# Performance work log

Hardware: AMD Instinct MI355X
Metric: run time of the kernel (lower is better)

## Reference

```python
import jax, jax.numpy as jnp
import numpy as np
import math

DIM = 147      # input feature dim
EMB = 64       # in_dim * head_cnt
M = 32         # int(EMB * kernel_ratio)
EPS_LN = 1e-5
EPS = 1e-8


def layer_norm(x, g, b, eps=EPS_LN):
    mu = jnp.mean(x, axis=-1, keepdims=True)
    var = jnp.mean(jnp.square(x - mu), axis=-1, keepdims=True)
    return (x - mu) * jax.lax.rsqrt(var + eps) * g + b


def prm_exp(x, W_rf):
    # x: [b, t, e], W_rf: [m, e]
    xd = 0.5 * jnp.sum(x * x, axis=-1, keepdims=True)        # [b, t, 1]
    wtx = jnp.einsum('bte,me->btm', x, W_rf)                  # [b, t, m]
    return jnp.exp(wtx - xd) / math.sqrt(M)


def setup_inputs() -> dict:
    key = jax.random.key(0)
    ks = jax.random.split(key, 16)
    B, T = 32, 3136
    s_in = 1.0 / math.sqrt(DIM)
    s_emb = 1.0 / math.sqrt(EMB)
    inp = {
        'x':      jax.random.normal(ks[0], (B, T, DIM), jnp.float32),
        'w_kqv':  jax.random.uniform(ks[1], (3 * EMB, DIM), jnp.float32, -s_in, s_in),
        'b_kqv':  jax.random.uniform(ks[2], (3 * EMB,), jnp.float32, -s_in, s_in),
        'w_proj': jax.random.uniform(ks[3], (EMB, EMB), jnp.float32, -s_emb, s_emb),
        'b_proj': jax.random.uniform(ks[4], (EMB,), jnp.float32, -s_emb, s_emb),
        'g1':     jnp.ones((DIM,), jnp.float32),
        'beta1':  jnp.zeros((DIM,), jnp.float32),
        'g2':     jnp.ones((EMB,), jnp.float32),
        'beta2':  jnp.zeros((EMB,), jnp.float32),
        'w_m1':   jax.random.uniform(ks[5], (EMB, EMB), jnp.float32, -s_emb, s_emb),
        'b_m1':   jax.random.uniform(ks[6], (EMB,), jnp.float32, -s_emb, s_emb),
        'w_m2':   jax.random.uniform(ks[7], (EMB, EMB), jnp.float32, -s_emb, s_emb),
        'b_m2':   jax.random.uniform(ks[8], (EMB,), jnp.float32, -s_emb, s_emb),
        # orthogonal random-feature matrix scaled by sqrt(m) (buffer 'w')
        'W_rf':   jnp.asarray(np.linalg.qr(np.random.RandomState(0).randn(EMB, EMB))[0][:M] * math.sqrt(M), jnp.float32),
    }
    return inp


def reference(x, w_kqv, b_kqv, w_proj, b_proj, g1, beta1, g2, beta2,
              w_m1, b_m1, w_m2, b_m2, W_rf):
    # --- single_attn(norm1(x)) ---
    xn = layer_norm(x, g1, beta1)
    kqv = xn @ w_kqv.T + b_kqv                                  # [b, t, 3e]
    k, q, v = jnp.split(kqv, 3, axis=-1)
    kp = prm_exp(k, W_rf)                                       # [b, t, m]
    qp = prm_exp(q, W_rf)                                       # [b, t, m]
    D = jnp.einsum('btm,bm->bt', qp, kp.sum(axis=1))[..., None]  # [b, t, 1]
    kptv = jnp.einsum('bte,btm->bem', v, kp)                    # [b, e, m]
    y = jnp.einsum('btm,bem->bte', qp, kptv) / (D + EPS)        # [b, t, e]
    y = v + (y @ w_proj.T + b_proj)                             # residual on v
    # --- y + mlp(norm2(y)) ---
    yn = layer_norm(y, g2, beta2)
    h = jax.nn.gelu(yn @ w_m1.T + b_m1, approximate=False)
    out = y + (h @ w_m2.T + b_m2)
    return out
```

## Files before the change

### kernel.cpp

```cpp
#include <hip/hip_runtime.h>
#include <hip/hip_bf16.h>

#define BB 32
#define TT 3136
#define DD 147
#define EE 64
#define MM 32
#define BT (BB*TT)

typedef __hip_bfloat16 bf16;
typedef __attribute__((ext_vector_type(8))) short s8v;
typedef __attribute__((ext_vector_type(4))) float f4v;

__device__ __forceinline__ float b2f(bf16 v){ return __bfloat162float(v); }
__device__ __forceinline__ bf16 f2b(float v){ return __float2bfloat16(v); }
__device__ __forceinline__ unsigned pack2(float a, float b){
  union { bf16 h[2]; unsigned u; } cv; cv.h[0]=f2b(a); cv.h[1]=f2b(b); return cv.u;
}

template<typename T>
__device__ __forceinline__ float cvt1(T v);
template<> __device__ __forceinline__ float cvt1<float>(float v){ return v; }
template<> __device__ __forceinline__ float cvt1<bf16>(bf16 v){ return __bfloat162float(v); }

__device__ __forceinline__ int bf16flag(const void* g1){
  return (*(const unsigned*)g1 == 0x3F803F80u) ? 1 : 0;
}

template<typename T>
__device__ void cvt_body(int idx,
    const T* wkqv, const T* bkqv, const T* Wrf, const T* wproj, const T* bproj,
    const T* g2, const T* be2, const T* wm1, const T* bm1, const T* wm2,
    const T* bm2, const T* g1, const T* be1,
    bf16* Bprep, bf16* WrfB, bf16* w0B, float* bprojF,
    float* g2F, float* be2F, bf16* w1B, float* bm1F, bf16* w2B,
    float* bm2F, float* c2F)
{
  if (idx < 30720){
    int n = idx/160, k = idx - n*160;
    Bprep[idx] = f2b(k < DD ? cvt1(wkqv[n*DD + k]) * cvt1(g1[k]) : 0.f);
    return;
  }
  idx -= 30720;
  if (idx < 2048){ WrfB[idx] = f2b(cvt1(Wrf[idx])); return; }
  idx -= 2048;
  if (idx < 4608){
    int e = idx/72, c = idx - e*72;
    w0B[idx] = f2b(c < 64 ? cvt1(wproj[e*64 + c]) : 0.f); return;
  }
  idx -= 4608;
  if (idx < 64){ bprojF[idx] = cvt1(bproj[idx]); return; }
  idx -= 64;
  if (idx < 64){ g2F[idx] = cvt1(g2[idx]); return; }
  idx -= 64;
  if (idx < 64){ be2F[idx] = cvt1(be2[idx]); return; }
  idx -= 64;
  if (idx < 4608){
    int e = idx/72, c = idx - e*72;
    w1B[idx] = f2b(c < 64 ? cvt1(wm1[e*64 + c]) : 0.f); return;
  }
  idx -= 4608;
  if (idx < 64){ bm1F[idx] = cvt1(bm1[idx]); return; }
  idx -= 64;
  if (idx < 4608){
    int e = idx/72, c = idx - e*72;
    w2B[idx] = f2b(c < 64 ? cvt1(wm2[e*64 + c]) : 0.f); return;
  }
  idx -= 4608;
  if (idx < 64){ bm2F[idx] = cvt1(bm2[idx]); return; }
  idx -= 64;
  if (idx < 12288){
    int n = idx>>6, ln = idx&63;
    float s = cvt1(wkqv[n*DD + ln])    * cvt1(be1[ln])
            + cvt1(wkqv[n*DD + 64+ln]) * cvt1(be1[64+ln]);
    if (ln < DD-128)
      s = fmaf(cvt1(wkqv[n*DD + 128+ln]), cvt1(be1[128+ln]), s);
    #pragma unroll
    for (int off=32; off; off>>=1) s += __shfl_xor(s, off);
    if (ln == 0) c2F[n] = s + cvt1(bkqv[n]);
    return;
  }
}

__global__ void k_cvt(const void* wkqv, const void* bkqv, const void* Wrf,
    const void* wproj, const void* bproj, const void* g2, const void* be2,
    const void* wm1, const void* bm1, const void* wm2, const void* bm2,
    const void* g1, const void* be1,
    bf16* Bprep, bf16* WrfB, bf16* w0B, float* bprojF,
    float* g2F, float* be2F, bf16* w1B, float* bm1F, bf16* w2B,
    float* bm2F, float* c2F,
    float* __restrict__ kptvF, float* __restrict__ ksumF)
{
  int idx = blockIdx.x*256 + threadIdx.x;
  if (idx < 65536) kptvF[idx] = 0.f;
  if (idx < 1024)  ksumF[idx] = 0.f;
  if (bf16flag(g1))
    cvt_body<bf16>(idx, (const bf16*)wkqv, (const bf16*)bkqv, (const bf16*)Wrf,
      (const bf16*)wproj, (const bf16*)bproj, (const bf16*)g2, (const bf16*)be2,
      (const bf16*)wm1, (const bf16*)bm1, (const bf16*)wm2, (const bf16*)bm2,
      (const bf16*)g1, (const bf16*)be1,
      Bprep, WrfB, w0B, bprojF, g2F, be2F, w1B, bm1F, w2B, bm2F, c2F);
  else
    cvt_body<float>(idx, (const float*)wkqv, (const float*)bkqv, (const float*)Wrf,
      (const float*)wproj, (const float*)bproj, (const float*)g2, (const float*)be2,
      (const float*)wm1, (const float*)bm1, (const float*)wm2, (const float*)bm2,
      (const float*)g1, (const float*)be1,
      Bprep, WrfB, w0B, bprojF, g2F, be2F, w1B, bm1F, w2B, bm2F, c2F);
}

__global__ __launch_bounds__(256,6) void k_a2(
    const void* __restrict__ x, const void* __restrict__ g1,
    const bf16* __restrict__ Bprep, const float* __restrict__ c2F,
    const bf16* __restrict__ WrfB,
    bf16* __restrict__ qp, bf16* __restrict__ v,
    float* __restrict__ kptvF, float* __restrict__ ksumF)
{
  __shared__ __align__(16) char smem[21504];
  bf16* vT   = (bf16*)smem;
  bf16* kpT  = (bf16*)(smem + 9216);

  int tid = threadIdx.x;
  size_t t0 = (size_t)blockIdx.x*64;
  int b = blockIdx.x / 49;

  int tw = tid>>6, lane = tid&63, quad = lane>>4, r = lane&15;
  int tRow = tw*16 + quad*4;
  char* strip = smem + tw*5376;
  bf16* lin = (bf16*)strip;
  bf16* aS  = (bf16*)strip;
  bf16* kqW = (bf16*)strip;

  if (bf16flag(g1)){
    const uint4* xg = (const uint4*)((const bf16*)x + (t0 + (size_t)tw*16)*DD);
    uint4* xo = (uint4*)lin;
    #pragma unroll
    for (int k=0; k<5; ++k){
      int c = k*64 + lane;
      if (c < 294) xo[c] = xg[c];
    }
  } else {
    const float4* xg = (const float4*)((const float*)x + (t0 + (size_t)tw*16)*DD);
    uint2* xo = (uint2*)lin;
    #pragma unroll
    for (int k=0; k<10; ++k){
      int c = k*64 + lane;
      if (c < 588){
        float4 f = xg[c];
        uint2 u; u.x = pack2(f.x, f.y); u.y = pack2(f.z, f.w);
        xo[c] = u;
      }
    }
  }

  int ti = lane>>2, sl = lane&3;
  const bf16* srow = lin + ti*DD;
  float xv[37];
  float s1 = 0.f, s2 = 0.f;
  #pragma unroll
  for (int j=0; j<37; ++j){
    int e = sl + 4*j;
    float vx = (e < DD) ? b2f(srow[e]) : 0.f;
    xv[j] = vx;
    s1 += vx;
    s2 = fmaf(vx, vx, s2);
  }
  s1 += __shfl_xor(s1,1); s1 += __shfl_xor(s1,2);
  s2 += __shfl_xor(s2,1); s2 += __shfl_xor(s2,2);
  float mu  = s1 * (1.f/147.f);
  float var = s2 * (1.f/147.f) - mu*mu;
  float rn  = rsqrtf(var + 1e-5f);

  bf16* arow = aS + ti*168;
  #pragma unroll
  for (int j=0; j<37; ++j){
    int e = sl + 4*j;
    if (e < DD)       arow[e] = f2b((xv[j]-mu)*rn);
    else if (e == DD) arow[e] = f2b(0.f);
  }
  arow[148+sl] = f2b(0.f); arow[152+sl] = f2b(0.f); arow[156+sl] = f2b(0.f);

  f4v zero = {0.f,0.f,0.f,0.f};

  f4v acc[12];
  #pragma unroll
  for (int nt=0; nt<12; ++nt) acc[nt] = zero;
  const bf16* aBase = aS + r*168 + quad*8;
  const bf16* bBase = &Bprep[r*160 + quad*8];
  #pragma unroll 1
  for (int ks=0; ks<5; ++ks){
    s8v a = *((const s8v*)(aBase + ks*32));
    #pragma unroll
    for (int nt=0; nt<12; ++nt){
      s8v bw = *((const s8v*)(bBase + nt*16*160 + ks*32));
      acc[nt] = __builtin_amdgcn_mfma_f32_16x16x32_bf16(a, bw, acc[nt], 0,0,0);
    }
  }

  float c2v[12];
  #pragma unroll
  for (int nt=0; nt<12; ++nt) c2v[nt] = c2F[nt*16 + r];

  float vv[4][4];
  #pragma unroll
  for (int nt=8; nt<12; ++nt){
    #pragma unroll
    for (int reg=0; reg<4; ++reg){
      vv[nt-8][reg] = acc[nt][reg] + c2v[nt];
      v[(t0 + tRow + reg)*64 + (nt-8)*16 + r] = f2b(vv[nt-8][reg]);
    }
  }

  float kq[8][4];
  #pragma unroll
  for (int nt=0; nt<8; ++nt)
    #pragma unroll
    for (int reg=0; reg<4; ++reg)
      kq[nt][reg] = acc[nt][reg] + c2v[nt];

  #pragma unroll
  for (int nt=0; nt<8; ++nt)
    #pragma unroll
    for (int reg=0; reg<4; ++reg)
      kqW[(quad*4+reg)*136 + nt*16 + r] = f2b(kq[nt][reg]);

  float xdk[4], xdq[4];
  #pragma unroll
  for (int reg=0; reg<4; ++reg){
    float sk = 0.f, sq = 0.f;
    #pragma unroll
    for (int nt=0; nt<4; ++nt){
      sk = fmaf(kq[nt][reg],   kq[nt][reg],   sk);
      sq = fmaf(kq[nt+4][reg], kq[nt+4][reg], sq);
    }
    #pragma unroll
    for (int off=1; off<16; off<<=1){
      sk += __shfl_xor(sk, off);
      sq += __shfl_xor(sq, off);
    }
    xdk[reg] = 0.5f*sk;
    xdq[reg] = 0.5f*sq;
  }

  f4v accP[2] = {zero, zero}, accQ[2] = {zero, zero};
  #pragma unroll
  for (int ks=0; ks<2; ++ks){
    s8v ak = *((const s8v*)&kqW[r*136 + ks*32 + quad*8]);
    s8v aq = *((const s8v*)&kqW[r*136 + 64 + ks*32 + quad*8]);
    #pragma unroll
    for (int nt=0; nt<2; ++nt){
      s8v wf = *((const s8v*)&WrfB[(nt*16+r)*64 + ks*32 + quad*8]);
      accP[nt] = __builtin_amdgcn_mfma_f32_16x16x32_bf16(ak, wf, accP[nt], 0,0,0);
      accQ[nt] = __builtin_amdgcn_mfma_f32_16x16x32_bf16(aq, wf, accQ[nt], 0,0,0);
    }
  }
  float kpv[2][4];
  #pragma unroll
  for (int nt=0; nt<2; ++nt){
    #pragma unroll
    for (int reg=0; reg<4; ++reg){
      size_t gt = t0 + tRow + reg;
      kpv[nt][reg] = expf(accP[nt][reg] - xdk[reg]) * 0.17677669529663687f;
      qp[gt*32 + nt*16 + r] = f2b(expf(accQ[nt][reg] - xdq[reg]) * 0.17677669529663687f);
    }
  }
  __syncthreads();

  #pragma unroll
  for (int nt=0; nt<4; ++nt){
    *((unsigned*)&vT[(nt*16+r)*72 + tRow])     = pack2(vv[nt][0], vv[nt][1]);
    *((unsigned*)&vT[(nt*16+r)*72 + tRow + 2]) = pack2(vv[nt][2], vv[nt][3]);
  }
  #pragma unroll
  for (int nt=0; nt<2; ++nt){
    *((unsigned*)&kpT[(nt*16+r)*72 + tRow])     = pack2(kpv[nt][0], kpv[nt][1]);
    *((unsigned*)&kpT[(nt*16+r)*72 + tRow + 2]) = pack2(kpv[nt][2], kpv[nt][3]);
  }

  float ks0 = kpv[0][0]+kpv[0][1]+kpv[0][2]+kpv[0][3];
  float ks1 = kpv[1][0]+kpv[1][1]+kpv[1][2]+kpv[1][3];
  ks0 += __shfl_xor(ks0, 16); ks0 += __shfl_xor(ks0, 32);
  ks1 += __shfl_xor(ks1, 16); ks1 += __shfl_xor(ks1, 32);
  if (lane < 16){
    atomicAdd(&ksumF[b*32 + r],      ks0);
    atomicAdd(&ksumF[b*32 + 16 + r], ks1);
  }
  __syncthreads();

  f4v accKV[2] = {zero, zero};
  #pragma unroll
  for (int kh=0; kh<2; ++kh){
    s8v av = *((const s8v*)&vT[(tw*16+r)*72 + kh*32 + quad*8]);
    #pragma unroll
    for (int nt=0; nt<2; ++nt){
      s8v bk = *((const s8v*)&kpT[(nt*16+r)*72 + kh*32 + quad*8]);
      accKV[nt] = __builtin_amdgcn_mfma_f32_16x16x32_bf16(av, bk, accKV[nt], 0,0,0);
    }
  }
  float* dst = kptvF + b*2048;
  #pragma unroll
  for (int nt=0; nt<2; ++nt)
    #pragma unroll
    for (int reg=0; reg<4; ++reg)
      atomicAdd(&dst[(tw*16 + quad*4 + reg)*32 + nt*16 + r], accKV[nt][reg]);
}

__global__ __launch_bounds__(256,4) void k_b(
    const bf16* __restrict__ qp, const bf16* __restrict__ v,
    const float* __restrict__ kptvF, const float* __restrict__ ksumF,
    const bf16* __restrict__ w0B, const float* __restrict__ bprojF,
    const float* __restrict__ g2F, const float* __restrict__ be2F,
    const bf16* __restrict__ w1B, const float* __restrict__ bm1F,
    const bf16* __restrict__ w2B, const float* __restrict__ bm2F,
    const void* __restrict__ g1, void* __restrict__ outp)
{
  __shared__ __align__(16) bf16 qpS[64*40];
  __shared__ __align__(16) bf16 kvS[64*40];
  __shared__ __align__(16) bf16 vS[64*72];
  __shared__ __align__(16) bf16 stA[64*72];
  __shared__ float ksS[32];
  __shared__ float bpS[64], b1S[64], b2S[64], gS[64], btS[64];

  int flag = bf16flag(g1);
  int tid = threadIdx.x;
  int b = blockIdx.y;
  int gt0 = b*TT + blockIdx.x*64;

  {
    int t = tid>>2, q = tid&3;
    uint4 u = ((const uint4*)(qp + (size_t)gt0*32))[tid];
    *((uint4*)&qpS[t*40 + q*8]) = u;
  }
  for (int i=tid; i<512; i+=256){
    int e = i>>3, q = i&7;
    float4 f = ((const float4*)(kptvF + b*2048))[i];
    union { bf16 h[4]; uint2 u; } cv;
    cv.h[0]=f2b(f.x); cv.h[1]=f2b(f.y); cv.h[2]=f2b(f.z); cv.h[3]=f2b(f.w);
    *((uint2*)&kvS[e*40 + q*4]) = cv.u;
  }
  for (int i=tid; i<512; i+=256){
    int t = i>>3, q = i&7;
    uint4 u = ((const uint4*)(v + (size_t)gt0*64))[i];
    *((uint4*)&vS[t*72 + q*8]) = u;
  }
  if (tid<32) ksS[tid] = ksumF[b*32+tid];
  if (tid<64){
    bpS[tid]=bprojF[tid]; b1S[tid]=bm1F[tid]; b2S[tid]=bm2F[tid];
    gS[tid]=g2F[tid]; btS[tid]=be2F[tid];
  }
  __syncthreads();

  int tw = tid>>6, lane = tid&63, quad = lane>>4, r = lane&15;
  int tRow = tw*16 + quad*4;
  f4v zero = {0.f,0.f,0.f,0.f};

  float dpart;
  {
    int ti = lane>>2, sl = lane&3;
    const bf16* qrow = &qpS[(tw*16+ti)*40];
    float s = 0.f;
    #pragma unroll
    for (int m=0; m<8; ++m) s = fmaf(b2f(qrow[sl*8+m]), ksS[sl*8+m], s);
    s += __shfl_xor(s,1); s += __shfl_xor(s,2);
    dpart = s;
  }
  float Dinv[4];
  #pragma unroll
  for (int reg=0; reg<4; ++reg){
    float d = __shfl(dpart, (lane & 0x30) + 4*reg);
    Dinv[reg] = 1.f/(d + 1e-8f);
  }

  f4v accA[4];
  {
    s8v aq = *((const s8v*)&qpS[(tw*16+r)*40 + quad*8]);
    #pragma unroll
    for (int nt=0; nt<4; ++nt){
      s8v bk = *((const s8v*)&kvS[(nt*16+r)*40 + quad*8]);
      accA[nt] = __builtin_amdgcn_mfma_f32_16x16x32_bf16(aq, bk, zero, 0,0,0);
    }
  }

  #pragma unroll
  for (int nt=0; nt<4; ++nt)
    #pragma unroll
    for (int reg=0; reg<4; ++reg)
      stA[(tRow+reg)*72 + nt*16 + r] = f2b(accA[nt][reg]*Dinv[reg]);

  f4v accY[4] = {zero, zero, zero, zero};
  #pragma unroll
  for (int kh=0; kh<2; ++kh){
    s8v ay = *((const s8v*)&stA[(tw*16+r)*72 + kh*32 + quad*8]);
    #pragma unroll
    for (int nt=0; nt<4; ++nt){
      s8v bw = *((const s8v*)&w0B[(nt*16+r)*72 + kh*32 + quad*8]);
      accY[nt] = __builtin_amdgcn_mfma_f32_16x16x32_bf16(ay, bw, accY[nt], 0,0,0);
    }
  }
  float y[4][4];
  #pragma unroll
  for (int nt=0; nt<4; ++nt){
    int e = nt*16 + r;
    float bp = bpS[e];
    #pragma unroll
    for (int reg=0; reg<4; ++reg)
      y[nt][reg] = accY[nt][reg] + b2f(vS[(tRow+reg)*72 + e]) + bp;
  }

  float mu[4], rs[4];
  #pragma unroll
  for (int reg=0; reg<4; ++reg){
    float s = y[0][reg]+y[1][reg]+y[2][reg]+y[3][reg];
    #pragma unroll
    for (int off=1; off<16; off<<=1) s += __shfl_xor(s, off);
    mu[reg] = s * (1.f/64.f);
  }
  #pragma unroll
  for (int reg=0; reg<4; ++reg){
    float d2 = 0.f;
    #pragma unroll
    for (int nt=0; nt<4; ++nt){ float d = y[nt][reg]-mu[reg]; d2 = fmaf(d,d,d2); }
    #pragma unroll
    for (int off=1; off<16; off<<=1) d2 += __shfl_xor(d2, off);
    rs[reg] = rsqrtf(d2*(1.f/64.f) + 1e-5f);
  }
  #pragma unroll
  for (int nt=0; nt<4; ++nt){
    int e = nt*16 + r;
    float g = gS[e], be = btS[e];
    #pragma unroll
    for (int reg=0; reg<4; ++reg)
      stA[(tRow+reg)*72 + e] = f2b((y[nt][reg]-mu[reg])*rs[reg]*g + be);
  }

  f4v accH[4] = {zero, zero, zero, zero};
  #pragma unroll
  for (int kh=0; kh<2; ++kh){
    s8v ah = *((const s8v*)&stA[(tw*16+r)*72 + kh*32 + quad*8]);
    #pragma unroll
    for (int nt=0; nt<4; ++nt){
      s8v bw = *((const s8v*)&w1B[(nt*16+r)*72 + kh*32 + quad*8]);
      accH[nt] = __builtin_amdgcn_mfma_f32_16x16x32_bf16(ah, bw, accH[nt], 0,0,0);
    }
  }
  #pragma unroll
  for (int nt=0; nt<4; ++nt){
    int e = nt*16 + r;
    float b1 = b1S[e];
    #pragma unroll
    for (int reg=0; reg<4; ++reg){
      float h = accH[nt][reg] + b1;
      h = 0.5f*h*(1.f + erff(h*0.70710678118654752f));
      stA[(tRow+reg)*72 + e] = f2b(h);
    }
  }

  f4v accO[4] = {zero, zero, zero, zero};
  #pragma unroll
  for (int kh=0; kh<2; ++kh){
    s8v ao = *((const s8v*)&stA[(tw*16+r)*72 + kh*32 + quad*8]);
    #pragma unroll
    for (int nt=0; nt<4; ++nt){
      s8v bw = *((const s8v*)&w2B[(nt*16+r)*72 + kh*32 + quad*8]);
      accO[nt] = __builtin_amdgcn_mfma_f32_16x16x32_bf16(ao, bw, accO[nt], 0,0,0);
    }
  }
  if (flag){
    bf16* o = (bf16*)outp;
    #pragma unroll
    for (int nt=0; nt<4; ++nt){
      int e = nt*16 + r;
      float b2 = b2S[e];
      #pragma unroll
      for (int reg=0; reg<4; ++reg)
        o[(size_t)(gt0 + tRow + reg)*64 + e] = f2b(y[nt][reg] + accO[nt][reg] + b2);
    }
  } else {
    float* o = (float*)outp;
    #pragma unroll
    for (int nt=0; nt<4; ++nt){
      int e = nt*16 + r;
      float b2 = b2S[e];
      #pragma unroll
      for (int reg=0; reg<4; ++reg)
        o[(size_t)(gt0 + tRow + reg)*64 + e] = y[nt][reg] + accO[nt][reg] + b2;
    }
  }
}

extern "C" void kernel_launch(void* const* d_in, const int* in_sizes, int n_in,
                              void* d_out, int out_size, void* d_ws, size_t ws_size,
                              hipStream_t stream){
  const void* x    = d_in[0];
  const void* wkqv = d_in[1];
  const void* bkqv = d_in[2];
  const void* wproj= d_in[3];
  const void* bproj= d_in[4];
  const void* g1   = d_in[5];
  const void* be1  = d_in[6];
  const void* g2   = d_in[7];
  const void* be2  = d_in[8];
  const void* wm1  = d_in[9];
  const void* bm1  = d_in[10];
  const void* wm2  = d_in[11];
  const void* bm2  = d_in[12];
  const void* Wrf  = d_in[13];

  char* ws = (char*)d_ws;
  bf16*  Bprep = (bf16*) (ws + 256);
  bf16*  WrfB  = (bf16*) (ws + 62464);
  bf16*  w0B   = (bf16*) (ws + 66560);
  float* bprojF= (float*)(ws + 82944);
  float* g2F   = (float*)(ws + 83200);
  float* be2F  = (float*)(ws + 83456);
  bf16*  w1B   = (bf16*) (ws + 83712);
  float* bm1F  = (float*)(ws + 100096);
  bf16*  w2B   = (bf16*) (ws + 100352);
  float* bm2F  = (float*)(ws + 116736);
  float* c2F   = (float*)(ws + 118784);
  float* kptvF = (float*)(ws + 32231424);
  float* ksumF = (float*)(ws + 32493568);
  bf16*  qp    = (bf16*) (ws + 32497664);
  bf16*  v     = (bf16*) (ws + 38920192);

  k_cvt<<<256, 256, 0, stream>>>(wkqv, bkqv, Wrf, wproj, bproj, g2, be2,
      wm1, bm1, wm2, bm2, g1, be1,
      Bprep, WrfB, w0B, bprojF, g2F, be2F, w1B, bm1F, w2B, bm2F,
      c2F, kptvF, ksumF);
  k_a2<<<BT/64, 256, 0, stream>>>(x, g1, Bprep, c2F, WrfB,
      qp, v, kptvF, ksumF);
  k_b<<<dim3(TT/64, BB), 256, 0, stream>>>(qp, v, kptvF, ksumF,
      w0B, bprojF, g2F, be2F, w1B, bm1F, w2B, bm2F, g1, d_out);
}
```

Baseline: 196.0 us.

## Replace global atomic reductions with per-block partials and a separate reduce kernel

Each k_a2 block now writes its kptv and ksum partial sums to a per-block workspace slot instead of issuing float atomicAdds into per-batch accumulators. A new k_red kernel sums the 49 partials per batch, and the zero-initialisation in k_cvt is removed. This targets contention from heavy atomic traffic, where 49 blocks hit the same 2048 addresses, at the cost of about 13MB of extra partial writes and reads plus one more launch. k_b launch bounds are also raised from 4 to 5 waves.

After: 193.6 us. No clear change (-1.2%).

```diff
diff --git a/kernel.cpp b/kernel.cpp
--- a/kernel.cpp
+++ b/kernel.cpp
@@ -88,12 +88,9 @@
     const void* g1, const void* be1,
     bf16* Bprep, bf16* WrfB, bf16* w0B, float* bprojF,
     float* g2F, float* be2F, bf16* w1B, float* bm1F, bf16* w2B,
-    float* bm2F, float* c2F,
-    float* __restrict__ kptvF, float* __restrict__ ksumF)
+    float* bm2F, float* c2F)
 {
   int idx = blockIdx.x*256 + threadIdx.x;
-  if (idx < 65536) kptvF[idx] = 0.f;
-  if (idx < 1024)  ksumF[idx] = 0.f;
   if (bf16flag(g1))
     cvt_body<bf16>(idx, (const bf16*)wkqv, (const bf16*)bkqv, (const bf16*)Wrf,
       (const bf16*)wproj, (const bf16*)bproj, (const bf16*)g2, (const bf16*)be2,
@@ -113,15 +110,15 @@
     const bf16* __restrict__ Bprep, const float* __restrict__ c2F,
     const bf16* __restrict__ WrfB,
     bf16* __restrict__ qp, bf16* __restrict__ v,
-    float* __restrict__ kptvF, float* __restrict__ ksumF)
+    float* __restrict__ kptvP, float* __restrict__ ksumP)
 {
   __shared__ __align__(16) char smem[21504];
+  __shared__ float ksumW[128];
   bf16* vT   = (bf16*)smem;
   bf16* kpT  = (bf16*)(smem + 9216);
 
   int tid = threadIdx.x;
   size_t t0 = (size_t)blockIdx.x*64;
-  int b = blockIdx.x / 49;
 
   int tw = tid>>6, lane = tid&63, quad = lane>>4, r = lane&15;
   int tRow = tw*16 + quad*4;
@@ -281,10 +278,14 @@
   ks0 += __shfl_xor(ks0, 16); ks0 += __shfl_xor(ks0, 32);
   ks1 += __shfl_xor(ks1, 16); ks1 += __shfl_xor(ks1, 32);
   if (lane < 16){
-    atomicAdd(&ksumF[b*32 + r],      ks0);
-    atomicAdd(&ksumF[b*32 + 16 + r], ks1);
+    ksumW[tw*32 + r]      = ks0;
+    ksumW[tw*32 + 16 + r] = ks1;
   }
   __syncthreads();
+
+  if (tid < 32)
+    ksumP[(size_t)blockIdx.x*32 + tid] =
+      ksumW[tid] + ksumW[32+tid] + ksumW[64+tid] + ksumW[96+tid];
 
   f4v accKV[2] = {zero, zero};
   #pragma unroll
@@ -296,15 +297,37 @@
       accKV[nt] = __builtin_amdgcn_mfma_f32_16x16x32_bf16(av, bk, accKV[nt], 0,0,0);
     }
   }
-  float* dst = kptvF + b*2048;
+  float* dst = kptvP + (size_t)blockIdx.x*2048;
   #pragma unroll
   for (int nt=0; nt<2; ++nt)
     #pragma unroll
     for (int reg=0; reg<4; ++reg)
-      atomicAdd(&dst[(tw*16 + quad*4 + reg)*32 + nt*16 + r], accKV[nt][reg]);
-}
-
-__global__ __launch_bounds__(256,4) void k_b(
+      dst[(tw*16 + quad*4 + reg)*32 + nt*16 + r] = accKV[nt][reg];
+}
+
+__global__ void k_red(const float* __restrict__ kptvP,
+                      const float* __restrict__ ksumP,
+                      float* __restrict__ kptvF, float* __restrict__ ksumF){
+  int idx = blockIdx.x*256 + threadIdx.x;
+  if (idx < 65536){
+    int b = idx >> 11, i = idx & 2047;
+    const float* src = kptvP + (size_t)b*49*2048 + i;
+    float s = 0.f;
+    #pragma unroll 7
+    for (int j=0; j<49; ++j) s += src[j*2048];
+    kptvF[idx] = s;
+  } else if (idx < 66560){
+    int k = idx - 65536;
+    int b = k >> 5, m = k & 31;
+    const float* src = ksumP + (size_t)b*49*32 + m;
+    float s = 0.f;
+    #pragma unroll 7
+    for (int j=0; j<49; ++j) s += src[j*32];
+    ksumF[k] = s;
+  }
+}
+
+__global__ __launch_bounds__(256,5) void k_b(
     const bf16* __restrict__ qp, const bf16* __restrict__ v,
     const float* __restrict__ kptvF, const float* __restrict__ ksumF,
     const bf16* __restrict__ w0B, const float* __restrict__ bprojF,
@@ -517,6 +540,8 @@
   bf16*  w2B   = (bf16*) (ws + 100352);
   float* bm2F  = (float*)(ws + 116736);
   float* c2F   = (float*)(ws + 118784);
+  float* kptvP = (float*)(ws + 131072);
+  float* ksumP = (float*)(ws + 12976128);
   float* kptvF = (float*)(ws + 32231424);
   float* ksumF = (float*)(ws + 32493568);
   bf16*  qp    = (bf16*) (ws + 32497664);
@@ -524,10 +549,10 @@
 
   k_cvt<<<256, 256, 0, stream>>>(wkqv, bkqv, Wrf, wproj, bproj, g2, be2,
       wm1, bm1, wm2, bm2, g1, be1,
-      Bprep, WrfB, w0B, bprojF, g2F, be2F, w1B, bm1F, w2B, bm2F,
-      c2F, kptvF, ksumF);
+      Bprep, WrfB, w0B, bprojF, g2F, be2F, w1B, bm1F, w2B, bm2F, c2F);
   k_a2<<<BT/64, 256, 0, stream>>>(x, g1, Bprep, c2F, WrfB,
-      qp, v, kptvF, ksumF);
+      qp, v, kptvP, ksumP);
+  k_red<<<260, 256, 0, stream>>>(kptvP, ksumP, kptvF, ksumF);
   k_b<<<dim3(TT/64, BB), 256, 0, stream>>>(qp, v, kptvF, ksumF,
       w0B, bprojF, g2F, be2F, w1B, bm1F, w2B, bm2F, g1, d_out);
 }
```
